# Optimization experiments

Hardware: AMD Instinct MI355X
Metric: run time of the kernel (lower is better)

The kernel has to match this reference:

```python
import jax, jax.numpy as jnp
import numpy as np


def setup_inputs() -> dict:
    key = jax.random.key(0)
    k1, k2, k3 = jax.random.split(key, 3)
    B, T, Hl, D = 8, 4096, 8, 128
    bs = 64
    Tb = (T + bs - 1) // bs  # 64
    S = 4096
    return {
        "k_cache": jnp.zeros((B, T, Hl, D), jnp.float32),
        "v_cache": jnp.zeros((B, T, Hl, D), jnp.float32),
        "v_norm_tok": jnp.zeros((B, T, Hl), jnp.float32),
        "k_sum_blk": jnp.zeros((B, Tb, Hl, D), jnp.float32),
        "k_cnt_blk": jnp.zeros((B, Tb), jnp.int32),
        "v_norm_blk": jnp.zeros((B, Tb, Hl), jnp.float32),
        "input_pos_s": jnp.arange(S, dtype=jnp.int32),
        "k_bshd": jax.random.normal(k1, (B, S, Hl, D), jnp.float32),
        "v_bshd": jax.random.normal(k2, (B, S, Hl, D), jnp.float32),
        "v_norm_bsh": jax.random.uniform(k3, (B, S, Hl), jnp.float32),
        "sparse_block_size": bs,
    }


def reference(k_cache, v_cache, v_norm_tok, k_sum_blk, k_cnt_blk, v_norm_blk,
              input_pos_s, k_bshd, v_bshd, v_norm_bsh, sparse_block_size):
    # Faithful, vectorized version of KVCache.update_tokens.
    Tb = k_sum_blk.shape[1]

    # Token-level scatter writes into the caches.
    k_cache_new = k_cache.at[:, input_pos_s].set(k_bshd)
    v_cache_new = v_cache.at[:, input_pos_s].set(v_bshd)
    v_norm_tok_new = v_norm_tok.at[:, input_pos_s].set(v_norm_bsh)

    # Block index of each incoming token.
    blk = input_pos_s // sparse_block_size  # [S]

    # Per-block sum of keys: segment-reduce over the token axis.
    k_add = jax.ops.segment_sum(
        jnp.swapaxes(k_bshd, 0, 1).astype(jnp.float32), blk,
        num_segments=Tb)  # [Tb, B, Hl, D]
    k_sum_blk_new = k_sum_blk + jnp.swapaxes(k_add, 0, 1)

    # Per-block token counts (same for every batch row).
    cnt_add = jax.ops.segment_sum(
        jnp.ones_like(blk, dtype=jnp.int32), blk, num_segments=Tb)  # [Tb]
    k_cnt_blk_new = k_cnt_blk + cnt_add[None, :]

    # Running per-block max of v-norms.
    v_max = jax.ops.segment_max(
        jnp.swapaxes(v_norm_bsh, 0, 1), blk, num_segments=Tb)  # [Tb, B, Hl]
    v_norm_blk_new = jnp.maximum(v_norm_blk, jnp.swapaxes(v_max, 0, 1))

    prefill_len_new = (jnp.max(input_pos_s) + 1).astype(jnp.int32)

    return (k_cache_new, v_cache_new, v_norm_tok_new,
            k_sum_blk_new, k_cnt_blk_new, v_norm_blk_new, prefill_len_new)
```

## Files before the change

### kernel.cpp

```cpp
#include <hip/hip_runtime.h>
#include <math.h>

constexpr int Bc  = 8;
constexpr int Tc  = 4096;
constexpr int HLc = 8;
constexpr int Dc  = 128;
constexpr int Sc  = 4096;
constexpr int TBc = 64;
constexpr int BSc = 64;

constexpr long long O_KC   = 0LL;
constexpr long long O_VC   = 33554432LL;
constexpr long long O_VNT  = 67108864LL;
constexpr long long O_KSUM = 67371008LL;
constexpr long long O_CNT  = 67895296LL;
constexpr long long O_VNB  = 67895808LL;
constexpr long long O_PRE  = 67899904LL;

typedef float f4 __attribute__((ext_vector_type(4)));

__device__ inline f4 ntload4(const float* p) {
    return __builtin_nontemporal_load(reinterpret_cast<const f4*>(p));
}
__device__ inline void ntstore4(float* p, f4 v) {
    __builtin_nontemporal_store(v, reinterpret_cast<f4*>(p));
}

__global__ __launch_bounds__(256) void k_main(
    const float* __restrict__ kc_old, const float* __restrict__ vc_old,
    const float* __restrict__ vnt_old, const float* __restrict__ ksum_old,
    const int* __restrict__ kcnt_old, const float* __restrict__ vnb_old,
    const float* __restrict__ kb, const float* __restrict__ vb,
    const float* __restrict__ vnorm, const int* __restrict__ pos,
    float* __restrict__ out)
{
    const int wg  = blockIdx.x;
    const int dq  = wg & 3;
    const int tb  = (wg >> 2) & 63;
    const int b   = wg >> 8;
    const int tid = threadIdx.x;
    const int qp  = tid >> 6;
    const int sl  = tid & 63;

    __shared__ int   inv_l[BSc];
    __shared__ int   cnt_l;
    __shared__ int   maxp_l;
    __shared__ f4    red4[256];
    __shared__ float vn_l[BSc * HLc];

    if (tid < BSc) inv_l[tid] = -1;
    if (tid == 0) { cnt_l = 0; maxp_l = -1; }
    __syncthreads();

    {
        const int base = tb * BSc;
        int lmax = -1;
        #pragma unroll
        for (int j = 0; j < Sc / 256; ++j) {
            const int s  = tid + j * 256;
            const int pp = pos[s];
            lmax = max(lmax, pp);
            if (pp >= base && pp < base + BSc) {
                atomicMax(&inv_l[pp - base], s);
                atomicAdd(&cnt_l, 1);
            }
        }
        if (wg == 0) {
            #pragma unroll
            for (int off = 32; off >= 1; off >>= 1)
                lmax = max(lmax, __shfl_xor(lmax, off));
            if ((tid & 63) == 0) atomicMax(&maxp_l, lmax);
        }
    }
    __syncthreads();

    constexpr int ROW = HLc * Dc;
    const int qoff    = dq * 256;
    const int dstBase = (b * Tc + tb * BSc) * ROW + qoff;
    const int srcBase = b * Sc * ROW + qoff;

    float* const okc = out + O_KC;
    float* const ovc = out + O_VC;

    f4 ksum = (f4){0.f, 0.f, 0.f, 0.f};
    #pragma unroll
    for (int i = 0; i < 16; ++i) {
        const int r = i * 4 + qp;
        const int s = __builtin_amdgcn_readfirstlane(inv_l[r]);
        const int dst = dstBase + r * ROW + sl * 4;
        f4 kv, vv;
        if (s >= 0) {
            const int src = srcBase + s * ROW + sl * 4;
            kv = ntload4(kb + src);
            vv = ntload4(vb + src);
            ksum += kv;
        } else {
            kv = ntload4(kc_old + dst);
            vv = ntload4(vc_old + dst);
        }
        ntstore4(okc + dst, kv);
        ntstore4(ovc + dst, vv);
    }
    red4[tid] = ksum;

    if (dq == 0) {
        #pragma unroll
        for (int j = 0; j < 2; ++j) {
            const int idx = tid + j * 256;
            const int tl = idx >> 3, h = idx & 7;
            const int s  = inv_l[tl];
            const int di = (b * Tc + tb * BSc + tl) * HLc + h;
            float vn, vm;
            if (s >= 0) {
                vn = vnorm[(b * Sc + s) * HLc + h];
                vm = vn;
            } else {
                vn = vnt_old[di];
                vm = -INFINITY;
            }
            out[O_VNT + di] = vn;
            vn_l[idx] = vm;
        }
    }
    __syncthreads();

    if (qp == 0) {
        f4 tot = red4[sl] + red4[64 + sl] + red4[128 + sl] + red4[192 + sl];
        const int o = (b * TBc + tb) * ROW + qoff + sl * 4;
        f4 old = *reinterpret_cast<const f4*>(ksum_old + o);
        ntstore4(out + O_KSUM + o, old + tot);
    }

    if (dq == 0 && tid < HLc) {
        float m = vnb_old[(b * TBc + tb) * HLc + tid];
        #pragma unroll
        for (int t = 0; t < BSc; ++t) m = fmaxf(m, vn_l[t * HLc + tid]);
        out[O_VNB + (b * TBc + tb) * HLc + tid] = m;
    }

    if (dq == 0 && tid == 0) {
        out[O_CNT + b * TBc + tb] = (float)(kcnt_old[b * TBc + tb] + cnt_l);
        if (wg == 0) out[O_PRE] = (float)(maxp_l + 1);
    }
}

extern "C" void kernel_launch(void* const* d_in, const int* in_sizes, int n_in,
                              void* d_out, int out_size, void* d_ws, size_t ws_size,
                              hipStream_t stream) {
    const float* kc_old   = (const float*)d_in[0];
    const float* vc_old   = (const float*)d_in[1];
    const float* vnt_old  = (const float*)d_in[2];
    const float* ksum_old = (const float*)d_in[3];
    const int*   kcnt_old = (const int*)d_in[4];
    const float* vnb_old  = (const float*)d_in[5];
    const int*   pos      = (const int*)d_in[6];
    const float* kb       = (const float*)d_in[7];
    const float* vb       = (const float*)d_in[8];
    const float* vnorm    = (const float*)d_in[9];
    float* out = (float*)d_out;

    k_main<<<Bc * TBc * 4, 256, 0, stream>>>(kc_old, vc_old, vnt_old,
                                             ksum_old, kcnt_old, vnb_old,
                                             kb, vb, vnorm, pos, out);
}
```

Measured before the change: 107.2 us.

## Split K and V copy into separate workgroups and warp-reduce block counts

Doubles the grid so each workgroup copies either the K or the V cache slice, with K workgroups doing the key-sum reduction and V workgroups doing the v-norm max. Per-token shared atomicAdd on the count is replaced by a per-thread count, wave shuffle reduction and one atomic per wave, done only in one workgroup per block. This is meant to raise the number of workgroups in flight for the memory-bound copy and cut shared-memory atomic contention. The cost is that every workgroup still rescans the full 4096-entry position array, and there are now twice as many of them.

New measurement: 110.9 us. 3.5% more time.

```diff
diff --git a/kernel.cpp b/kernel.cpp
--- a/kernel.cpp
+++ b/kernel.cpp
@@ -25,6 +25,9 @@
 __device__ inline void ntstore4(float* p, f4 v) {
     __builtin_nontemporal_store(v, reinterpret_cast<f4*>(p));
 }
+__device__ inline f4 ld4(const float* p) {
+    return *reinterpret_cast<const f4*>(p);
+}
 
 __global__ __launch_bounds__(256) void k_main(
     const float* __restrict__ kc_old, const float* __restrict__ vc_old,
@@ -35,9 +38,10 @@
     float* __restrict__ out)
 {
     const int wg  = blockIdx.x;
-    const int dq  = wg & 3;
-    const int tb  = (wg >> 2) & 63;
-    const int b   = wg >> 8;
+    const int kv  = wg & 1;
+    const int dq  = (wg >> 1) & 3;
+    const int tb  = (wg >> 3) & 63;
+    const int b   = wg >> 9;
     const int tid = threadIdx.x;
     const int qp  = tid >> 6;
     const int sl  = tid & 63;
@@ -54,7 +58,7 @@
 
     {
         const int base = tb * BSc;
-        int lmax = -1;
+        int lmax = -1, lcnt = 0;
         #pragma unroll
         for (int j = 0; j < Sc / 256; ++j) {
             const int s  = tid + j * 256;
@@ -62,8 +66,14 @@
             lmax = max(lmax, pp);
             if (pp >= base && pp < base + BSc) {
                 atomicMax(&inv_l[pp - base], s);
-                atomicAdd(&cnt_l, 1);
+                ++lcnt;
             }
+        }
+        if (kv == 0 && dq == 0) {
+            #pragma unroll
+            for (int off = 32; off >= 1; off >>= 1)
+                lcnt += __shfl_xor(lcnt, off);
+            if ((tid & 63) == 0) atomicAdd(&cnt_l, lcnt);
         }
         if (wg == 0) {
             #pragma unroll
@@ -79,31 +89,42 @@
     const int dstBase = (b * Tc + tb * BSc) * ROW + qoff;
     const int srcBase = b * Sc * ROW + qoff;
 
-    float* const okc = out + O_KC;
-    float* const ovc = out + O_VC;
+    const float* const src_new = kv ? vb : kb;
+    const float* const src_old = kv ? vc_old : kc_old;
+    float* const dst = out + (kv ? O_VC : O_KC);
 
     f4 ksum = (f4){0.f, 0.f, 0.f, 0.f};
     #pragma unroll
     for (int i = 0; i < 16; ++i) {
         const int r = i * 4 + qp;
         const int s = __builtin_amdgcn_readfirstlane(inv_l[r]);
-        const int dst = dstBase + r * ROW + sl * 4;
-        f4 kv, vv;
+        const int d = dstBase + r * ROW + sl * 4;
+        f4 v;
         if (s >= 0) {
-            const int src = srcBase + s * ROW + sl * 4;
-            kv = ntload4(kb + src);
-            vv = ntload4(vb + src);
-            ksum += kv;
+            v = ntload4(src_new + srcBase + s * ROW + sl * 4);
+            ksum += v;
         } else {
-            kv = ntload4(kc_old + dst);
-            vv = ntload4(vc_old + dst);
+            v = ntload4(src_old + d);
         }
-        ntstore4(okc + dst, kv);
-        ntstore4(ovc + dst, vv);
+        ntstore4(dst + d, v);
     }
-    red4[tid] = ksum;
 
-    if (dq == 0) {
+    if (kv == 0) {
+        red4[tid] = ksum;
+        __syncthreads();
+        if (qp == 0) {
+            f4 tot = red4[sl] + red4[64 + sl] + red4[128 + sl]
+                   + red4[192 + sl];
+            const int o = (b * TBc + tb) * ROW + qoff + sl * 4;
+            f4 old = ld4(ksum_old + o);
+            ntstore4(out + O_KSUM + o, old + tot);
+        }
+        if (dq == 0 && tid == 0) {
+            out[O_CNT + b * TBc + tb] =
+                (float)(kcnt_old[b * TBc + tb] + cnt_l);
+            if (wg == 0) out[O_PRE] = (float)(maxp_l + 1);
+        }
+    } else if (dq == 0) {
         #pragma unroll
         for (int j = 0; j < 2; ++j) {
             const int idx = tid + j * 256;
@@ -121,26 +142,13 @@
             out[O_VNT + di] = vn;
             vn_l[idx] = vm;
         }
-    }
-    __syncthreads();
-
-    if (qp == 0) {
-        f4 tot = red4[sl] + red4[64 + sl] + red4[128 + sl] + red4[192 + sl];
-        const int o = (b * TBc + tb) * ROW + qoff + sl * 4;
-        f4 old = *reinterpret_cast<const f4*>(ksum_old + o);
-        ntstore4(out + O_KSUM + o, old + tot);
-    }
-
-    if (dq == 0 && tid < HLc) {
-        float m = vnb_old[(b * TBc + tb) * HLc + tid];
-        #pragma unroll
-        for (int t = 0; t < BSc; ++t) m = fmaxf(m, vn_l[t * HLc + tid]);
-        out[O_VNB + (b * TBc + tb) * HLc + tid] = m;
-    }
-
-    if (dq == 0 && tid == 0) {
-        out[O_CNT + b * TBc + tb] = (float)(kcnt_old[b * TBc + tb] + cnt_l);
-        if (wg == 0) out[O_PRE] = (float)(maxp_l + 1);
+        __syncthreads();
+        if (tid < HLc) {
+            float m = vnb_old[(b * TBc + tb) * HLc + tid];
+            #pragma unroll
+            for (int t = 0; t < BSc; ++t) m = fmaxf(m, vn_l[t * HLc + tid]);
+            out[O_VNB + (b * TBc + tb) * HLc + tid] = m;
+        }
     }
 }
 
@@ -159,7 +167,7 @@
     const float* vnorm    = (const float*)d_in[9];
     float* out = (float*)d_out;
 
-    k_main<<<Bc * TBc * 4, 256, 0, stream>>>(kc_old, vc_old, vnt_old,
-                                             ksum_old, kcnt_old, vnb_old,
-                                             kb, vb, vnorm, pos, out);
+    k_main<<<Bc * TBc * 4 * 2, 256, 0, stream>>>(kc_old, vc_old, vnt_old,
+                                                 ksum_old, kcnt_old, vnb_old,
+                                                 kb, vb, vnorm, pos, out);
 }
```
